# Kernel tuning notes

Measured on AMD Instinct MI355X. Metric: run time of the kernel, lower is better.

Reference implementation:

```python
import jax, jax.numpy as jnp
import numpy as np

B, T, D_MODEL, HEAD_DIM = 16, 4096, 512, 64


def setup_inputs() -> dict:
    key = jax.random.key(0)
    kx, kq, kk, kv = jax.random.split(key, 4)
    x = jax.random.normal(kx, (B, T, D_MODEL), dtype=jnp.float32)
    # torch nn.Linear weights, stored pre-transposed as [in, out] for x @ W
    s = 1.0 / np.sqrt(D_MODEL)
    Wq = jax.random.uniform(kq, (D_MODEL, HEAD_DIM), jnp.float32, -s, s)
    Wk = jax.random.uniform(kk, (D_MODEL, HEAD_DIM), jnp.float32, -s, s)
    Wv = jax.random.uniform(kv, (D_MODEL, HEAD_DIM), jnp.float32, -s, s)
    return {"x": x, "Wq": Wq, "Wk": Wk, "Wv": Wv}


def reference(x, Wq, Wk, Wv):
    # Single-head causal self-attention (dropout in eval mode = identity)
    q = x @ Wq  # [B, T, h]
    k = x @ Wk
    v = x @ Wv
    scale = 1.0 / np.sqrt(HEAD_DIM).astype(np.float32)
    scores = jnp.einsum("bth,bsh->bts", q, k) * scale  # [B, T, T]
    t = scores.shape[1]
    causal = jnp.tril(jnp.ones((t, t), dtype=bool))
    scores = jnp.where(causal, scores, -jnp.inf)
    weights = jax.nn.softmax(scores, axis=-1)
    return jnp.einsum("bts,bsh->bth", weights, v)  # [B, T, h]
```

## Files before the change

kernel.cpp:

```cpp
#include <hip/hip_runtime.h>
#include <hip/hip_bf16.h>
#include <math.h>


#define NB 16
#define NT 4096
#define DMODEL 512
#define HD 64
#define CEXP 0.18033688011112042f

typedef unsigned short u16;
typedef unsigned int u32;
typedef __attribute__((ext_vector_type(2))) unsigned int u32x2;
typedef __attribute__((ext_vector_type(8))) short bf16x8;
typedef __attribute__((ext_vector_type(4))) float f32x4;
typedef __attribute__((ext_vector_type(16))) float f32x16;

__device__ __forceinline__ u16 bfu(float x) {
  __hip_bfloat16 h = __float2bfloat16(x);
  return *(u16*)&h;
}

__device__ __forceinline__ u32 cvtpk(float lo, float hi) {
  u32 r;
  asm("v_cvt_pk_bf16_f32 %0, %1, %2" : "=v"(r) : "v"(lo), "v"(hi));
  return r;
}

__device__ __forceinline__ u32x2 lane_swap(u32 a, u32 b) {
  asm("v_permlane32_swap_b32 %0, %1" : "+v"(a), "+v"(b));
  u32x2 r; r[0] = a; r[1] = b; return r;
}

__device__ __forceinline__ void gload16(const void* g, void* l) {
  __builtin_amdgcn_global_load_lds(
      (const __attribute__((address_space(1))) void*)g,
      (__attribute__((address_space(3))) void*)l, 16, 0, 0);
}

#define MFMA32(a, b, c) __builtin_amdgcn_mfma_f32_16x16x32_bf16(a, b, c, 0, 0, 0)
#define WMFMA(a, b, c)  __builtin_amdgcn_mfma_f32_32x32x16_bf16(a, b, c, 0, 0, 0)
#define LD8(p) (*(const bf16x8*)(p))

__global__ void prep_wt(const float* __restrict__ Wq, const float* __restrict__ Wk,
                        const float* __restrict__ Wv, u16* __restrict__ Wt) {
  int k0 = blockIdx.x * 16;
  int t = threadIdx.x;
#pragma unroll
  for (int i = 0; i < 12; ++i) {
    int idx = t + i * 256;
    int n = idx % 192;
    int kk = idx / 192;
    const float* W = (n < 64) ? Wq : (n < 128) ? Wk : Wv;
    float w = W[(size_t)(k0 + kk) * 64 + (n & 63)];
    Wt[(size_t)n * 512 + k0 + kk] = bfu(w);
  }
}

__global__ __launch_bounds__(512) void proj_qkv(const float* __restrict__ x,
                                                const u16* __restrict__ Wt,
                                                u16* __restrict__ qo,
                                                u16* __restrict__ ko,
                                                u16* __restrict__ vo) {
  __shared__ u16 As[2][128][48];
  int t = threadIdx.x;
  int m0 = blockIdx.x * 128;
  int lane = t & 63, wid = t >> 6;
  int wr = wid >> 2, wc = wid & 3;
  int g = lane >> 4, li = lane & 15;
  f32x4 acc[4][3];
#pragma unroll
  for (int i = 0; i < 4; ++i)
#pragma unroll
    for (int j = 0; j < 3; ++j) acc[i][j] = (f32x4){0.f, 0.f, 0.f, 0.f};

  int row = t >> 2, quad = t & 3;
  const float* srcb = x + (size_t)(m0 + row) * DMODEL + quad * 8;

  float4 pa0[3], pa1[3];
#pragma unroll
  for (int s = 0; s < 3; ++s) {
    pa0[s] = *(const float4*)(srcb + s * 32);
    pa1[s] = *(const float4*)(srcb + s * 32 + 4);
  }

#pragma unroll
  for (int s = 0; s < 16; ++s) {
    float4 c0 = pa0[s % 3], c1 = pa1[s % 3];
    if (s + 3 < 16) {
      pa0[s % 3] = *(const float4*)(srcb + (s + 3) * 32);
      pa1[s % 3] = *(const float4*)(srcb + (s + 3) * 32 + 4);
    }
    union { u16 u[8]; bf16x8 v; } tmp;
    tmp.u[0] = bfu(c0.x); tmp.u[1] = bfu(c0.y);
    tmp.u[2] = bfu(c0.z); tmp.u[3] = bfu(c0.w);
    tmp.u[4] = bfu(c1.x); tmp.u[5] = bfu(c1.y);
    tmp.u[6] = bfu(c1.z); tmp.u[7] = bfu(c1.w);
    *(bf16x8*)&As[s & 1][row][quad * 8] = tmp.v;
    __syncthreads();

    int k0 = s * 32;
    bf16x8 a[4], bb[3];
#pragma unroll
    for (int mf = 0; mf < 4; ++mf)
      a[mf] = *(const bf16x8*)&As[s & 1][wr * 64 + mf * 16 + li][g * 8];
#pragma unroll
    for (int nf = 0; nf < 3; ++nf)
      bb[nf] = *(const bf16x8*)(Wt + (size_t)(wc * 48 + nf * 16 + li) * 512 + k0 + g * 8);
#pragma unroll
    for (int mf = 0; mf < 4; ++mf)
#pragma unroll
      for (int nf = 0; nf < 3; ++nf)
        acc[mf][nf] = MFMA32(a[mf], bb[nf], acc[mf][nf]);
  }

#pragma unroll
  for (int nf = 0; nf < 3; ++nf) {
    int n = wc * 48 + nf * 16 + li;
    if (n < 64) {
      int col = n;
#pragma unroll
      for (int mf = 0; mf < 4; ++mf)
#pragma unroll
        for (int r = 0; r < 4; ++r) {
          int m = m0 + wr * 64 + mf * 16 + 4 * g + r;
          qo[(size_t)m * HD + col] = bfu(acc[mf][nf][r] * CEXP);
        }
    } else if (n < 128) {
      int col = n & 63;
      int dt = col >> 4, hh = (col >> 3) & 1, jj = col & 7;
      size_t fo = (size_t)(dt * 2 + hh) * 256 + jj;
#pragma unroll
      for (int mf = 0; mf < 4; ++mf)
#pragma unroll
        for (int r = 0; r < 4; ++r) {
          int m = m0 + wr * 64 + mf * 16 + 4 * g + r;
          ko[(size_t)(m >> 5) * 2048 + fo + (m & 31) * 8] = bfu(acc[mf][nf][r]);
        }
    } else {
      int d = n - 128;
      int dh = d >> 5, l31d = d & 31;
#pragma unroll
      for (int mf = 0; mf < 4; ++mf) {
        int mbase = m0 + wr * 64 + mf * 16 + 4 * g;
        int kk2 = mbase & 31;
        int kt2 = kk2 >> 4, hh = (kk2 >> 3) & 1;
        size_t off = (size_t)(mbase >> 5) * 2048 +
                     (size_t)((dh * 2 + kt2) * 2 + hh) * 256 + l31d * 8 + (mbase & 7);
        ushort4 pk;
        pk.x = bfu(acc[mf][nf][0]);
        pk.y = bfu(acc[mf][nf][1]);
        pk.z = bfu(acc[mf][nf][2]);
        pk.w = bfu(acc[mf][nf][3]);
        *(ushort4*)(vo + off) = pk;
      }
    }
  }
}

__global__ __launch_bounds__(256, 3) void attn_fwd14(const u16* __restrict__ qg,
                                                     const u16* __restrict__ kg,
                                                     const u16* __restrict__ vg,
                                                     float* __restrict__ out) {
  __shared__ __align__(16) char smem[32768];
  u16* KV = (u16*)smem;
  float* MrgF = (float*)smem;

  int tid = threadIdx.x;
  int lane = tid & 63, w = tid >> 6;
  int l31 = lane & 31, h = lane >> 5;
  int qi = w >> 1, ki = w & 1;

  int f = blockIdx.x;
  int xcd = f & 7, i = f >> 3;
  int b = 2 * xcd + (i & 1);
  int bp = 63 - (i >> 1);

  const int limb = 2 * bp + 1;
  const int diagw = 2 * bp + qi;
  const int nr = (bp + 2) >> 1;
  const int q0w = bp * 64 + qi * 32;

  const u16* qb = qg + (size_t)b * NT * HD;
  const u16* kbs = kg + (size_t)b * NT * HD;
  const u16* vbs = vg + (size_t)b * NT * HD;
  float* ob = out + (size_t)b * NT * HD;

  bf16x8 qf[4];
#pragma unroll
  for (int dt = 0; dt < 4; ++dt)
    qf[dt] = LD8(qb + (size_t)(q0w + l31) * HD + dt * 16 + 8 * h);

  f32x16 oacc0, oacc1;
#pragma unroll
  for (int r = 0; r < 16; ++r) { oacc0[r] = 0.f; oacc1[r] = 0.f; }
  float lsum = 0.f;

  auto STAGEK = [&](u16* lb, int tg) {
    const u16* gk = kbs + (size_t)tg * 2048 + lane * 8;
    u16* dk = lb + w * 2048 + lane * 8;
#pragma unroll
    for (int ii = 0; ii < 4; ++ii)
      gload16(gk + ii * 512, dk + ii * 512);
  };
  auto LOADV = [&](bf16x8 (&vf)[4], int jj) {
    const u16* vp = vbs + (size_t)jj * 2048 + h * 256 + l31 * 8;
#pragma unroll
    for (int dv = 0; dv < 4; ++dv)
      vf[dv] = LD8(vp + dv * 512);
  };

  auto COMPUTE = [&](const u16* kp0, const bf16x8 (&vf)[4], bool maskdiag) {
    bf16x8 kf[4];
#pragma unroll
    for (int dt = 0; dt < 4; ++dt)
      kf[dt] = LD8(kp0 + dt * 512 + h * 256 + l31 * 8);

    f32x16 sv;
#pragma unroll
    for (int r = 0; r < 16; ++r) sv[r] = 0.f;
    sv = WMFMA(kf[0], qf[0], sv);
    sv = WMFMA(kf[1], qf[1], sv);
    sv = WMFMA(kf[2], qf[2], sv);
    sv = WMFMA(kf[3], qf[3], sv);

    if (maskdiag) {
#pragma unroll
      for (int r = 0; r < 16; ++r) {
        int key = (r & 3) + 8 * (r >> 2) + 4 * h;
        if (key > l31) sv[r] = -1e30f;
      }
    }

    float p[16];
#pragma unroll
    for (int r = 0; r < 16; ++r) p[r] = __builtin_amdgcn_exp2f(sv[r]);
    lsum += (((p[0] + p[1]) + (p[2] + p[3])) + ((p[4] + p[5]) + (p[6] + p[7]))) +
            (((p[8] + p[9]) + (p[10] + p[11])) + ((p[12] + p[13]) + (p[14] + p[15])));
    u32 A0 = cvtpk(p[0], p[1]),   A1 = cvtpk(p[2], p[3]);
    u32 B0 = cvtpk(p[4], p[5]),   B1 = cvtpk(p[6], p[7]);
    u32 C0 = cvtpk(p[8], p[9]),   C1 = cvtpk(p[10], p[11]);
    u32 E0 = cvtpk(p[12], p[13]), E1 = cvtpk(p[14], p[15]);
    u32x2 s0 = lane_swap(A0, B0), s1 = lane_swap(A1, B1);
    u32x2 s2 = lane_swap(C0, E0), s3 = lane_swap(C1, E1);
    union { u32 d[4]; bf16x8 v; } f0u, f1u;
    f0u.d[0] = s0[0]; f0u.d[1] = s1[0]; f0u.d[2] = s0[1]; f0u.d[3] = s1[1];
    f1u.d[0] = s2[0]; f1u.d[1] = s3[0]; f1u.d[2] = s2[1]; f1u.d[3] = s3[1];

    oacc0 = WMFMA(vf[0], f0u.v, oacc0);
    oacc1 = WMFMA(vf[2], f0u.v, oacc1);
    oacc0 = WMFMA(vf[1], f1u.v, oacc0);
    oacc1 = WMFMA(vf[3], f1u.v, oacc1);
  };

  STAGEK(KV, min(w, limb));

  int cur = 0;
  for (int jr = 0; jr < nr; ++jr) {
    int j1 = 4 * jr + ki, j2 = 4 * jr + 2 + ki;
    bf16x8 vf1[4], vf2[4];
    LOADV(vf1, min(j1, 127));
    LOADV(vf2, min(j2, 127));
    if (jr + 1 < nr) {
      STAGEK(KV + (cur ^ 1) * 8192, min(4 * (jr + 1) + w, limb));
      asm volatile("s_waitcnt vmcnt(12)" ::: "memory");
    } else {
      asm volatile("s_waitcnt vmcnt(8)" ::: "memory");
    }
    __builtin_amdgcn_sched_barrier(0);
    asm volatile("s_barrier" ::: "memory");

    const u16* kv0 = KV + cur * 8192;
    __builtin_amdgcn_s_setprio(1);
    if (j1 <= diagw) COMPUTE(kv0 + ki * 2048, vf1, j1 == diagw);
    if (j2 <= diagw) COMPUTE(kv0 + (2 + ki) * 2048, vf2, j2 == diagw);
    __builtin_amdgcn_s_setprio(0);

    asm volatile("s_barrier" ::: "memory");
    cur ^= 1;
  }

  lsum += __shfl_xor(lsum, 32);
#pragma unroll
  for (int s = 0; s < 2; ++s) {
    if (s) __syncthreads();
    {
      float* mg = MrgF + ((size_t)w * 64 + lane) * 17;
      const f32x16& oS = s ? oacc1 : oacc0;
#pragma unroll
      for (int r = 0; r < 16; ++r) mg[r] = oS[r];
      mg[16] = lsum;
    }
    __syncthreads();
    const float* m0p = MrgF + ((size_t)(qi * 2) * 64) * 17;
    const float* m1p = MrgF + ((size_t)(qi * 2 + 1) * 64) * 17;
#pragma unroll
    for (int t2 = 0; t2 < 2; ++t2) {
      int ql = (lane >> 2) + 16 * t2;
      float ls = m0p[(size_t)ql * 17 + 16] + m1p[(size_t)ql * 17 + 16];
      float inv = 1.0f / ls;
      f32x4 o4;
#pragma unroll
      for (int dd = 0; dd < 4; ++dd) {
        int rem = ki * 16 + (lane & 3) * 4 + dd;
        int srch = (rem >> 2) & 1;
        int reg = (rem & 3) + ((rem >> 3) << 2);
        size_t ro = (size_t)(ql + 32 * srch) * 17 + reg;
        o4[dd] = (m0p[ro] + m1p[ro]) * inv;
      }
      int d0 = s * 32 + ki * 16 + (lane & 3) * 4;
      *(f32x4*)(ob + (size_t)(q0w + ql) * HD + d0) = o4;
    }
  }
}

extern "C" void kernel_launch(void* const* d_in, const int* in_sizes, int n_in,
                              void* d_out, int out_size, void* d_ws, size_t ws_size,
                              hipStream_t stream) {
  const float* x  = (const float*)d_in[0];
  const float* Wq = (const float*)d_in[1];
  const float* Wk = (const float*)d_in[2];
  const float* Wv = (const float*)d_in[3];
  float* out = (float*)d_out;

  u16* Wt  = (u16*)d_ws;
  u16* qws = (u16*)((char*)d_ws + 192 * 512 * 2);
  u16* kws = qws + (size_t)NB * NT * HD;
  u16* vws = kws + (size_t)NB * NT * HD;

  prep_wt<<<32, 256, 0, stream>>>(Wq, Wk, Wv, Wt);
  proj_qkv<<<(NB * NT) / 128, 512, 0, stream>>>(x, Wt, qws, kws, vws);
  attn_fwd14<<<1024, 256, 0, stream>>>(qws, kws, vws, out);
}
```

Baseline: 93.68 us.

## Use 512-thread blocks with 128-query tiles and stage K and V in LDS

```diff
diff --git a/kernel.cpp b/kernel.cpp
--- a/kernel.cpp
+++ b/kernel.cpp
@@ -158,11 +158,11 @@
   }
 }
 
-__global__ __launch_bounds__(256, 3) void attn_fwd14(const u16* __restrict__ qg,
+__global__ __launch_bounds__(512, 4) void attn_fwd18(const u16* __restrict__ qg,
                                                      const u16* __restrict__ kg,
                                                      const u16* __restrict__ vg,
                                                      float* __restrict__ out) {
-  __shared__ __align__(16) char smem[32768];
+  __shared__ __align__(16) char smem[65536];
   u16* KV = (u16*)smem;
   float* MrgF = (float*)smem;
 
@@ -173,13 +173,14 @@
 
   int f = blockIdx.x;
   int xcd = f & 7, i = f >> 3;
-  int b = 2 * xcd + (i & 1);
-  int bp = 63 - (i >> 1);
-
-  const int limb = 2 * bp + 1;
-  const int diagw = 2 * bp + qi;
-  const int nr = (bp + 2) >> 1;
-  const int q0w = bp * 64 + qi * 32;
+  int b, bp;
+  if (i < 32) { b = 2 * xcd;     bp = 31 - i; }
+  else        { b = 2 * xcd + 1; bp = i - 32; }
+
+  const int limb = 4 * bp + 3;
+  const int diagw = 4 * bp + qi;
+  const int nr = bp + 1;
+  const int q0w = bp * 128 + qi * 32;
 
   const u16* qb = qg + (size_t)b * NT * HD;
   const u16* kbs = kg + (size_t)b * NT * HD;
@@ -196,25 +197,24 @@
   for (int r = 0; r < 16; ++r) { oacc0[r] = 0.f; oacc1[r] = 0.f; }
   float lsum = 0.f;
 
-  auto STAGEK = [&](u16* lb, int tg) {
-    const u16* gk = kbs + (size_t)tg * 2048 + lane * 8;
-    u16* dk = lb + w * 2048 + lane * 8;
+  auto STAGE = [&](u16* lb, int jr1) {
+    int t4 = w >> 1, part = w & 1;
+    int tg = min(4 * jr1 + t4, limb);
+    const u16* gsrc = (part ? vbs : kbs) + (size_t)tg * 2048 + lane * 8;
+    u16* dk = lb + t4 * 4096 + part * 2048 + lane * 8;
 #pragma unroll
     for (int ii = 0; ii < 4; ++ii)
-      gload16(gk + ii * 512, dk + ii * 512);
+      gload16(gsrc + ii * 512, dk + ii * 512);
   };
-  auto LOADV = [&](bf16x8 (&vf)[4], int jj) {
-    const u16* vp = vbs + (size_t)jj * 2048 + h * 256 + l31 * 8;
-#pragma unroll
-    for (int dv = 0; dv < 4; ++dv)
-      vf[dv] = LD8(vp + dv * 512);
-  };
-
-  auto COMPUTE = [&](const u16* kp0, const bf16x8 (&vf)[4], bool maskdiag) {
-    bf16x8 kf[4];
+
+  auto COMPUTE = [&](const u16* kp0, const u16* vp0, bool maskdiag) {
+    bf16x8 kf[4], vf[4];
 #pragma unroll
     for (int dt = 0; dt < 4; ++dt)
       kf[dt] = LD8(kp0 + dt * 512 + h * 256 + l31 * 8);
+#pragma unroll
+    for (int dv = 0; dv < 4; ++dv)
+      vf[dv] = LD8(vp0 + dv * 512 + h * 256 + l31 * 8);
 
     f32x16 sv;
 #pragma unroll
@@ -253,27 +253,26 @@
     oacc1 = WMFMA(vf[3], f1u.v, oacc1);
   };
 
-  STAGEK(KV, min(w, limb));
+  STAGE(KV, 0);
 
   int cur = 0;
   for (int jr = 0; jr < nr; ++jr) {
-    int j1 = 4 * jr + ki, j2 = 4 * jr + 2 + ki;
-    bf16x8 vf1[4], vf2[4];
-    LOADV(vf1, min(j1, 127));
-    LOADV(vf2, min(j2, 127));
     if (jr + 1 < nr) {
-      STAGEK(KV + (cur ^ 1) * 8192, min(4 * (jr + 1) + w, limb));
-      asm volatile("s_waitcnt vmcnt(12)" ::: "memory");
+      STAGE(KV + (cur ^ 1) * 16384, jr + 1);
+      asm volatile("s_waitcnt vmcnt(4)" ::: "memory");
     } else {
-      asm volatile("s_waitcnt vmcnt(8)" ::: "memory");
+      asm volatile("s_waitcnt vmcnt(0)" ::: "memory");
     }
     __builtin_amdgcn_sched_barrier(0);
     asm volatile("s_barrier" ::: "memory");
 
-    const u16* kv0 = KV + cur * 8192;
+    const u16* kv0 = KV + cur * 16384;
+    int j1 = 4 * jr + ki, j2 = 4 * jr + 2 + ki;
     __builtin_amdgcn_s_setprio(1);
-    if (j1 <= diagw) COMPUTE(kv0 + ki * 2048, vf1, j1 == diagw);
-    if (j2 <= diagw) COMPUTE(kv0 + (2 + ki) * 2048, vf2, j2 == diagw);
+    if (j1 <= diagw)
+      COMPUTE(kv0 + ki * 4096, kv0 + ki * 4096 + 2048, j1 == diagw);
+    if (j2 <= diagw)
+      COMPUTE(kv0 + (2 + ki) * 4096, kv0 + (2 + ki) * 4096 + 2048, j2 == diagw);
     __builtin_amdgcn_s_setprio(0);
 
     asm volatile("s_barrier" ::: "memory");
@@ -283,7 +282,7 @@
   lsum += __shfl_xor(lsum, 32);
 #pragma unroll
   for (int s = 0; s < 2; ++s) {
-    if (s) __syncthreads();
+    __syncthreads();
     {
       float* mg = MrgF + ((size_t)w * 64 + lane) * 17;
       const f32x16& oS = s ? oacc1 : oacc0;
@@ -330,5 +329,5 @@
 
   prep_wt<<<32, 256, 0, stream>>>(Wq, Wk, Wv, Wt);
   proj_qkv<<<(NB * NT) / 128, 512, 0, stream>>>(x, Wt, qws, kws, vws);
-  attn_fwd14<<<1024, 256, 0, stream>>>(qws, kws, vws, out);
-}
+  attn_fwd18<<<512, 512, 0, stream>>>(qws, kws, vws, out);
+}
```

New measurement: 90.45 us. 1.04x faster.
